# Optimization experiments

Hardware: AMD Instinct MI355X
Metric: run time of the kernel (lower is better)

The kernel has to match this reference:

```python
import jax, jax.numpy as jnp
import numpy as np

NU = 1.0  # degrees of freedom of the Student-t / Tsallis softmax


def setup_inputs() -> dict:
    key = jax.random.key(0)
    k1, k2, k3, k4 = jax.random.split(key, 4)
    B, Nx, Nh, Ny = 8192, 2048, 512, 1024
    x = jax.random.normal(k1, (B, Nx), dtype=jnp.float32)
    W_fc = jax.random.normal(k2, (Nh, Nx), dtype=jnp.float32) * (1.0 / np.sqrt(Nx))
    b_fc = jax.random.normal(k3, (Nh,), dtype=jnp.float32) * 0.01
    W_q = jax.random.normal(k4, (Ny, Nh), dtype=jnp.float32) * (1.0 / np.sqrt(Nh))
    return {"x": x, "W_fc": W_fc, "b_fc": b_fc, "W_q": W_q}


def reference(x, W_fc, b_fc, W_q):
    # x: [B, Nx] -> relu -> Linear(Nx, Nh) -> relu
    h = jax.nn.relu(jax.nn.relu(x) @ W_fc.T + b_fc)  # [B, Nh]
    # Quadratic layer: squared Euclidean distance to each class prototype.
    # ||h - w_j||^2 = ||h||^2 - 2 h.w_j + ||w_j||^2  (avoids [B, Ny, Nh] tensor)
    d = (jnp.sum(h * h, axis=-1, keepdims=True)
         - 2.0 * (h @ W_q.T)
         + jnp.sum(W_q * W_q, axis=-1))  # [B, Ny]
    d = jnp.maximum(d, 0.0)  # guard tiny negatives from fp cancellation
    # LogTSoftmax: p_j \propto (1 + d_j/nu)^{-(nu+1)/2}
    t = (-(NU + 1.0) / 2.0) * jnp.log1p(d / NU)  # [B, Ny]
    return t - jax.scipy.special.logsumexp(t, axis=-1, keepdims=True)
```

## Files before the change

kernel.cpp:

```cpp
#include <hip/hip_runtime.h>
#include <stdint.h>
#include <stddef.h>

#define B_ROWS 8192
#define NX 2048
#define NH 512
#define NY 1024

typedef __attribute__((ext_vector_type(8))) short bf16x8;
typedef __attribute__((ext_vector_type(4))) short bf16x4;
typedef __attribute__((ext_vector_type(4))) float f32x4;

static __device__ __forceinline__ unsigned short f2bf(float f) {
    union { float f; unsigned int u; } c; c.f = f;
    unsigned int r = 0x7FFFu + ((c.u >> 16) & 1u);
    return (unsigned short)((c.u + r) >> 16);
}
static __device__ __forceinline__ float bf2f(unsigned short b) {
    union { unsigned int u; float f; } c; c.u = ((unsigned int)b) << 16;
    return c.f;
}

static __device__ __forceinline__ void glld16(const void* g, void* l) {
    __builtin_amdgcn_global_load_lds(
        (const __attribute__((address_space(1))) unsigned int*)g,
        (__attribute__((address_space(3))) unsigned int*)l, 16, 0, 0);
}


__global__ __launch_bounds__(256) void cast_x_kernel(const float* __restrict__ x,
                                                     unsigned short* __restrict__ xb) {
    size_t idx = (size_t)(blockIdx.x * 256 + threadIdx.x) * 8;
    float4 a = *(const float4*)&x[idx];
    float4 b = *(const float4*)&x[idx + 4];
    bf16x8 o;
    o[0] = (short)f2bf(fmaxf(a.x, 0.f)); o[1] = (short)f2bf(fmaxf(a.y, 0.f));
    o[2] = (short)f2bf(fmaxf(a.z, 0.f)); o[3] = (short)f2bf(fmaxf(a.w, 0.f));
    o[4] = (short)f2bf(fmaxf(b.x, 0.f)); o[5] = (short)f2bf(fmaxf(b.y, 0.f));
    o[6] = (short)f2bf(fmaxf(b.z, 0.f)); o[7] = (short)f2bf(fmaxf(b.w, 0.f));
    *(bf16x8*)&xb[idx] = o;
}

__global__ __launch_bounds__(256) void cast_wfc_kernel(const float* __restrict__ w,
                                                       unsigned short* __restrict__ wb) {
    int idx = (blockIdx.x * 256 + threadIdx.x) * 4;
    float4 v = *(const float4*)&w[idx];
    bf16x4 o;
    o[0] = (short)f2bf(v.x); o[1] = (short)f2bf(v.y);
    o[2] = (short)f2bf(v.z); o[3] = (short)f2bf(v.w);
    *(bf16x4*)&wb[idx] = o;
}

__global__ __launch_bounds__(256) void prep_wq_kernel(const float* __restrict__ wq,
                                                      unsigned short* __restrict__ wqb,
                                                      float* __restrict__ wqsq) {
    int lane = threadIdx.x & 63;
    int row = blockIdx.x * 4 + (threadIdx.x >> 6);
    const float* p = wq + (size_t)row * NH + lane * 8;
    float4 a = *(const float4*)p;
    float4 b = *(const float4*)(p + 4);
    bf16x8 o;
    o[0] = (short)f2bf(a.x); o[1] = (short)f2bf(a.y);
    o[2] = (short)f2bf(a.z); o[3] = (short)f2bf(a.w);
    o[4] = (short)f2bf(b.x); o[5] = (short)f2bf(b.y);
    o[6] = (short)f2bf(b.z); o[7] = (short)f2bf(b.w);
    *(bf16x8*)&wqb[(size_t)row * NH + lane * 8] = o;
    float s = a.x*a.x + a.y*a.y + a.z*a.z + a.w*a.w
            + b.x*b.x + b.y*b.y + b.z*b.z + b.w*b.w;
    #pragma unroll
    for (int off = 32; off > 0; off >>= 1) s += __shfl_xor(s, off);
    if (lane == 0) wqsq[row] = s;
}

__global__ __launch_bounds__(256, 2) void gemm1_kernel(const unsigned short* __restrict__ xb,
                                                       const unsigned short* __restrict__ wfcb,
                                                       const float* __restrict__ b_fc,
                                                       unsigned short* __restrict__ hb) {
    __shared__ unsigned short As[64 * 64];
    __shared__ unsigned short Bs[128 * 64];

    const int tid = threadIdx.x;
    const int lane = tid & 63;
    const int wave = tid >> 6;
    const int wm = wave >> 1, wn = wave & 1;
    const int quad = lane >> 4;
    const int r = lane & 15;
    const int m0 = blockIdx.y * 64;
    const int n0 = blockIdx.x * 128;

    f32x4 acc[2][4];
    #pragma unroll
    for (int i = 0; i < 2; ++i)
        #pragma unroll
        for (int j = 0; j < 4; ++j) acc[i][j] = (f32x4)(0.0f);

    const int lrow = lane >> 3;
    const int gch = (lane & 7) ^ lrow;
    const char* xbB = (const char*)xb;
    const char* wfB = (const char*)wfcb;
    char* AsB = (char*)As;
    char* BsB = (char*)Bs;

    const int xk = r & 7;
    const int ch0 = ((quad) ^ xk) * 16;
    const int ch1 = ((4 + quad) ^ xk) * 16;
    const char* ardp = AsB + (wm * 32 + r) * 128;
    const char* brdp = BsB + (wn * 64 + r) * 128;

    for (int k0 = 0; k0 < NX; k0 += 64) {
        __syncthreads();
        #pragma unroll
        for (int c = 0; c < 2; ++c) {
            int R0 = wave * 16 + c * 8;
            glld16(xbB + (size_t)(m0 + R0 + lrow) * (NX * 2) + k0 * 2 + gch * 16,
                   AsB + R0 * 128);
        }
        #pragma unroll
        for (int c = 0; c < 4; ++c) {
            int R0 = wave * 32 + c * 8;
            glld16(wfB + (size_t)(n0 + R0 + lrow) * (NX * 2) + k0 * 2 + gch * 16,
                   BsB + R0 * 128);
        }
        __syncthreads();

        #pragma unroll
        for (int s = 0; s < 2; ++s) {
            const int ch = s ? ch1 : ch0;
            bf16x8 af[2], bfv[4];
            #pragma unroll
            for (int i = 0; i < 2; ++i) af[i] = *(const bf16x8*)(ardp + i * 16 * 128 + ch);
            #pragma unroll
            for (int j = 0; j < 4; ++j) bfv[j] = *(const bf16x8*)(brdp + j * 16 * 128 + ch);
            #pragma unroll
            for (int i = 0; i < 2; ++i)
                #pragma unroll
                for (int j = 0; j < 4; ++j)
                    acc[i][j] = __builtin_amdgcn_mfma_f32_16x16x32_bf16(af[i], bfv[j], acc[i][j], 0, 0, 0);
        }
    }

    #pragma unroll
    for (int i = 0; i < 2; ++i) {
        #pragma unroll
        for (int j = 0; j < 4; ++j) {
            int col = n0 + wn * 64 + j * 16 + r;
            float bias = b_fc[col];
            #pragma unroll
            for (int rr = 0; rr < 4; ++rr) {
                int row = m0 + wm * 32 + i * 16 + quad * 4 + rr;
                float v = fmaxf(acc[i][j][rr] + bias, 0.0f);
                hb[(size_t)row * NH + col] = f2bf(v);
            }
        }
    }
}

__global__ __launch_bounds__(256) void hsq_kernel(const unsigned short* __restrict__ hb,
                                                  float* __restrict__ hsq) {
    int lane = threadIdx.x & 63;
    int row = blockIdx.x * 4 + (threadIdx.x >> 6);
    bf16x8 v = *(const bf16x8*)&hb[(size_t)row * NH + lane * 8];
    float s = 0.f;
    #pragma unroll
    for (int i = 0; i < 8; ++i) {
        float f = bf2f((unsigned short)v[i]);
        s += f * f;
    }
    #pragma unroll
    for (int off = 32; off > 0; off >>= 1) s += __shfl_xor(s, off);
    if (lane == 0) hsq[row] = s;
}

__global__ __launch_bounds__(256, 2) void gemm2_kernel(const unsigned short* __restrict__ hb,
                                                       const unsigned short* __restrict__ wqb,
                                                       const float* __restrict__ hsq,
                                                       const float* __restrict__ wqsq,
                                                       float* __restrict__ out) {
    __shared__ unsigned short As[128 * 64];
    __shared__ unsigned short Bs[128 * 64];

    const int tid = threadIdx.x;
    const int lane = tid & 63;
    const int wave = tid >> 6;
    const int wm = wave >> 1, wn = wave & 1;
    const int quad = lane >> 4;
    const int r = lane & 15;
    const int m0 = blockIdx.y * 128;
    const int n0 = blockIdx.x * 128;

    f32x4 acc[4][4];
    #pragma unroll
    for (int i = 0; i < 4; ++i)
        #pragma unroll
        for (int j = 0; j < 4; ++j) acc[i][j] = (f32x4)(0.0f);

    const int lrow = lane >> 3;
    const int gch = (lane & 7) ^ lrow;
    const char* hbB = (const char*)hb;
    const char* wqB = (const char*)wqb;
    char* AsB = (char*)As;
    char* BsB = (char*)Bs;

    const int xk = r & 7;
    const int ch0 = ((quad) ^ xk) * 16;
    const int ch1 = ((4 + quad) ^ xk) * 16;
    const char* ardp = AsB + (wm * 64 + r) * 128;
    const char* brdp = BsB + (wn * 64 + r) * 128;

    for (int k0 = 0; k0 < NH; k0 += 64) {
        __syncthreads();
        #pragma unroll
        for (int c = 0; c < 4; ++c) {
            int R0 = wave * 32 + c * 8;
            glld16(hbB + (size_t)(m0 + R0 + lrow) * (NH * 2) + k0 * 2 + gch * 16,
                   AsB + R0 * 128);
            glld16(wqB + (size_t)(n0 + R0 + lrow) * (NH * 2) + k0 * 2 + gch * 16,
                   BsB + R0 * 128);
        }
        __syncthreads();

        #pragma unroll
        for (int s = 0; s < 2; ++s) {
            const int ch = s ? ch1 : ch0;
            bf16x8 af[4], bfv[4];
            #pragma unroll
            for (int i = 0; i < 4; ++i) af[i] = *(const bf16x8*)(ardp + i * 16 * 128 + ch);
            #pragma unroll
            for (int j = 0; j < 4; ++j) bfv[j] = *(const bf16x8*)(brdp + j * 16 * 128 + ch);
            #pragma unroll
            for (int i = 0; i < 4; ++i)
                #pragma unroll
                for (int j = 0; j < 4; ++j)
                    acc[i][j] = __builtin_amdgcn_mfma_f32_16x16x32_bf16(af[i], bfv[j], acc[i][j], 0, 0, 0);
        }
    }

    float hs[4][4];
    #pragma unroll
    for (int i = 0; i < 4; ++i)
        #pragma unroll
        for (int rr = 0; rr < 4; ++rr)
            hs[i][rr] = hsq[m0 + wm * 64 + i * 16 + quad * 4 + rr];

    #pragma unroll
    for (int i = 0; i < 4; ++i) {
        #pragma unroll
        for (int j = 0; j < 4; ++j) {
            int col = n0 + wn * 64 + j * 16 + r;
            float wq = wqsq[col];
            #pragma unroll
            for (int rr = 0; rr < 4; ++rr) {
                int row = m0 + wm * 64 + i * 16 + quad * 4 + rr;
                float d = hs[i][rr] - 2.0f * acc[i][j][rr] + wq;
                d = fmaxf(d, 0.0f);
                out[(size_t)row * NY + col] = -__logf(1.0f + d);
            }
        }
    }
}

__global__ __launch_bounds__(256) void lse_kernel(float* __restrict__ out) {
    __shared__ float redm[4];
    __shared__ float reds[4];
    const int tid = threadIdx.x;
    const int lane = tid & 63;
    const int wave = tid >> 6;
    float* p = out + (size_t)blockIdx.x * NY;
    float4 v = ((const float4*)p)[tid];
    float m = fmaxf(fmaxf(v.x, v.y), fmaxf(v.z, v.w));
    #pragma unroll
    for (int off = 32; off > 0; off >>= 1) m = fmaxf(m, __shfl_xor(m, off));
    if (lane == 0) redm[wave] = m;
    __syncthreads();
    m = fmaxf(fmaxf(redm[0], redm[1]), fmaxf(redm[2], redm[3]));
    float s = __expf(v.x - m) + __expf(v.y - m) + __expf(v.z - m) + __expf(v.w - m);
    #pragma unroll
    for (int off = 32; off > 0; off >>= 1) s += __shfl_xor(s, off);
    if (lane == 0) reds[wave] = s;
    __syncthreads();
    s = reds[0] + reds[1] + reds[2] + reds[3];
    float lse = m + __logf(s);
    v.x -= lse; v.y -= lse; v.z -= lse; v.w -= lse;
    ((float4*)p)[tid] = v;
}

extern "C" void kernel_launch(void* const* d_in, const int* in_sizes, int n_in,
                              void* d_out, int out_size, void* d_ws, size_t ws_size,
                              hipStream_t stream) {
    const float* x    = (const float*)d_in[0];
    const float* W_fc = (const float*)d_in[1];
    const float* b_fc = (const float*)d_in[2];
    const float* W_q  = (const float*)d_in[3];
    float* out = (float*)d_out;

    char* ws = (char*)d_ws;
    unsigned short* xb   = (unsigned short*)(ws);
    unsigned short* wfcb = (unsigned short*)(ws + 33554432);
    unsigned short* wqb  = (unsigned short*)(ws + 35651584);
    float*          wqsq = (float*)(ws + 36700160);
    unsigned short* hb   = (unsigned short*)(ws + 36704256);
    float*          hsq  = (float*)(ws + 45092864);

    cast_x_kernel<<<(B_ROWS * NX) / (256 * 8), 256, 0, stream>>>(x, xb);
    cast_wfc_kernel<<<(NH * NX) / (256 * 4), 256, 0, stream>>>(W_fc, wfcb);
    prep_wq_kernel<<<NY / 4, 256, 0, stream>>>(W_q, wqb, wqsq);
    gemm1_kernel<<<dim3(NH / 128, B_ROWS / 64), 256, 0, stream>>>(xb, wfcb, b_fc, hb);
    hsq_kernel<<<B_ROWS / 4, 256, 0, stream>>>(hb, hsq);
    gemm2_kernel<<<dim3(NY / 128, B_ROWS / 128), 256, 0, stream>>>(hb, wqb, hsq, wqsq, out);
    lse_kernel<<<B_ROWS, 256, 0, stream>>>(out);
}
```

Before: 183.0 us.

## Merge prep kernels, fuse row norms into GEMM1, deepen K tiles, simplify LSE

The three cast/prep kernels become one launch, and that launch also zeroes the hsq buffer. The ||h||^2 row sums are now accumulated in the GEMM1 epilogue with shuffles and atomicAdd, so the separate hsq kernel and its re-read of h go away. Both GEMMs now stage 128-wide K slices per barrier pair (doubling LDS per block), and GEMM1's launch bounds ask for 3 blocks per CU. The log-sum-exp drops its max reduction and one barrier, relying on all logits being non-positive. The costs are atomics, float rounding that now differs slightly from the bf16-rounded h, and higher LDS use that may limit occupancy.

```diff
diff --git a/kernel.cpp b/kernel.cpp
--- a/kernel.cpp
+++ b/kernel.cpp
@@ -7,6 +7,11 @@
 #define NH 512
 #define NY 1024
 
+#define X_ELEMS (B_ROWS * NX)
+#define EW_ELEMS (X_ELEMS + NH * NX)
+#define EW_BLOCKS (EW_ELEMS / (8 * 256))
+#define WQ_BLOCKS (NY / 4)
+
 typedef __attribute__((ext_vector_type(8))) short bf16x8;
 typedef __attribute__((ext_vector_type(4))) short bf16x4;
 typedef __attribute__((ext_vector_type(4))) float f32x4;
@@ -16,10 +21,6 @@
     unsigned int r = 0x7FFFu + ((c.u >> 16) & 1u);
     return (unsigned short)((c.u + r) >> 16);
 }
-static __device__ __forceinline__ float bf2f(unsigned short b) {
-    union { unsigned int u; float f; } c; c.u = ((unsigned int)b) << 16;
-    return c.f;
-}
 
 static __device__ __forceinline__ void glld16(const void* g, void* l) {
     __builtin_amdgcn_global_load_lds(
@@ -27,57 +28,67 @@
         (__attribute__((address_space(3))) unsigned int*)l, 16, 0, 0);
 }
 
-
-__global__ __launch_bounds__(256) void cast_x_kernel(const float* __restrict__ x,
-                                                     unsigned short* __restrict__ xb) {
-    size_t idx = (size_t)(blockIdx.x * 256 + threadIdx.x) * 8;
-    float4 a = *(const float4*)&x[idx];
-    float4 b = *(const float4*)&x[idx + 4];
-    bf16x8 o;
-    o[0] = (short)f2bf(fmaxf(a.x, 0.f)); o[1] = (short)f2bf(fmaxf(a.y, 0.f));
-    o[2] = (short)f2bf(fmaxf(a.z, 0.f)); o[3] = (short)f2bf(fmaxf(a.w, 0.f));
-    o[4] = (short)f2bf(fmaxf(b.x, 0.f)); o[5] = (short)f2bf(fmaxf(b.y, 0.f));
-    o[6] = (short)f2bf(fmaxf(b.z, 0.f)); o[7] = (short)f2bf(fmaxf(b.w, 0.f));
-    *(bf16x8*)&xb[idx] = o;
-}
-
-__global__ __launch_bounds__(256) void cast_wfc_kernel(const float* __restrict__ w,
-                                                       unsigned short* __restrict__ wb) {
-    int idx = (blockIdx.x * 256 + threadIdx.x) * 4;
-    float4 v = *(const float4*)&w[idx];
-    bf16x4 o;
-    o[0] = (short)f2bf(v.x); o[1] = (short)f2bf(v.y);
-    o[2] = (short)f2bf(v.z); o[3] = (short)f2bf(v.w);
-    *(bf16x4*)&wb[idx] = o;
-}
-
-__global__ __launch_bounds__(256) void prep_wq_kernel(const float* __restrict__ wq,
-                                                      unsigned short* __restrict__ wqb,
-                                                      float* __restrict__ wqsq) {
-    int lane = threadIdx.x & 63;
-    int row = blockIdx.x * 4 + (threadIdx.x >> 6);
-    const float* p = wq + (size_t)row * NH + lane * 8;
-    float4 a = *(const float4*)p;
-    float4 b = *(const float4*)(p + 4);
-    bf16x8 o;
-    o[0] = (short)f2bf(a.x); o[1] = (short)f2bf(a.y);
-    o[2] = (short)f2bf(a.z); o[3] = (short)f2bf(a.w);
-    o[4] = (short)f2bf(b.x); o[5] = (short)f2bf(b.y);
-    o[6] = (short)f2bf(b.z); o[7] = (short)f2bf(b.w);
-    *(bf16x8*)&wqb[(size_t)row * NH + lane * 8] = o;
-    float s = a.x*a.x + a.y*a.y + a.z*a.z + a.w*a.w
-            + b.x*b.x + b.y*b.y + b.z*b.z + b.w*b.w;
-    #pragma unroll
-    for (int off = 32; off > 0; off >>= 1) s += __shfl_xor(s, off);
-    if (lane == 0) wqsq[row] = s;
-}
-
-__global__ __launch_bounds__(256, 2) void gemm1_kernel(const unsigned short* __restrict__ xb,
+__global__ __launch_bounds__(256) void prep_kernel(const float* __restrict__ x,
+                                                   const float* __restrict__ wfc,
+                                                   const float* __restrict__ wq,
+                                                   unsigned short* __restrict__ xb,
+                                                   unsigned short* __restrict__ wfcb,
+                                                   unsigned short* __restrict__ wqb,
+                                                   float* __restrict__ wqsq,
+                                                   float* __restrict__ hsq) {
+    const int bid = blockIdx.x;
+    const int tid = threadIdx.x;
+    if (bid < EW_BLOCKS) {
+        size_t idx = ((size_t)bid * 256 + tid) * 8;
+        if (idx < (size_t)X_ELEMS) {
+            float4 a = *(const float4*)&x[idx];
+            float4 b = *(const float4*)&x[idx + 4];
+            bf16x8 o;
+            o[0] = (short)f2bf(fmaxf(a.x, 0.f)); o[1] = (short)f2bf(fmaxf(a.y, 0.f));
+            o[2] = (short)f2bf(fmaxf(a.z, 0.f)); o[3] = (short)f2bf(fmaxf(a.w, 0.f));
+            o[4] = (short)f2bf(fmaxf(b.x, 0.f)); o[5] = (short)f2bf(fmaxf(b.y, 0.f));
+            o[6] = (short)f2bf(fmaxf(b.z, 0.f)); o[7] = (short)f2bf(fmaxf(b.w, 0.f));
+            *(bf16x8*)&xb[idx] = o;
+        } else {
+            size_t off = idx - X_ELEMS;
+            float4 a = *(const float4*)&wfc[off];
+            float4 b = *(const float4*)&wfc[off + 4];
+            bf16x8 o;
+            o[0] = (short)f2bf(a.x); o[1] = (short)f2bf(a.y);
+            o[2] = (short)f2bf(a.z); o[3] = (short)f2bf(a.w);
+            o[4] = (short)f2bf(b.x); o[5] = (short)f2bf(b.y);
+            o[6] = (short)f2bf(b.z); o[7] = (short)f2bf(b.w);
+            *(bf16x8*)&wfcb[off] = o;
+        }
+    } else {
+        const int b2 = bid - EW_BLOCKS;
+        const int lane = tid & 63;
+        const int row = b2 * 4 + (tid >> 6);
+        const float* p = wq + (size_t)row * NH + lane * 8;
+        float4 a = *(const float4*)p;
+        float4 b = *(const float4*)(p + 4);
+        bf16x8 o;
+        o[0] = (short)f2bf(a.x); o[1] = (short)f2bf(a.y);
+        o[2] = (short)f2bf(a.z); o[3] = (short)f2bf(a.w);
+        o[4] = (short)f2bf(b.x); o[5] = (short)f2bf(b.y);
+        o[6] = (short)f2bf(b.z); o[7] = (short)f2bf(b.w);
+        *(bf16x8*)&wqb[(size_t)row * NH + lane * 8] = o;
+        float s = a.x*a.x + a.y*a.y + a.z*a.z + a.w*a.w
+                + b.x*b.x + b.y*b.y + b.z*b.z + b.w*b.w;
+        #pragma unroll
+        for (int off = 32; off > 0; off >>= 1) s += __shfl_xor(s, off);
+        if (lane == 0) wqsq[row] = s;
+        if (tid < 32) hsq[b2 * 32 + tid] = 0.0f;
+    }
+}
+
+__global__ __launch_bounds__(256, 3) void gemm1_kernel(const unsigned short* __restrict__ xb,
                                                        const unsigned short* __restrict__ wfcb,
                                                        const float* __restrict__ b_fc,
-                                                       unsigned short* __restrict__ hb) {
-    __shared__ unsigned short As[64 * 64];
-    __shared__ unsigned short Bs[128 * 64];
+                                                       unsigned short* __restrict__ hb,
+                                                       float* __restrict__ hsq) {
+    __shared__ unsigned short As[2 * 64 * 64];
+    __shared__ unsigned short Bs[2 * 128 * 64];
 
     const int tid = threadIdx.x;
     const int lane = tid & 63;
@@ -107,37 +118,52 @@
     const char* ardp = AsB + (wm * 32 + r) * 128;
     const char* brdp = BsB + (wn * 64 + r) * 128;
 
-    for (int k0 = 0; k0 < NX; k0 += 64) {
+    for (int k0 = 0; k0 < NX; k0 += 128) {
         __syncthreads();
         #pragma unroll
-        for (int c = 0; c < 2; ++c) {
-            int R0 = wave * 16 + c * 8;
-            glld16(xbB + (size_t)(m0 + R0 + lrow) * (NX * 2) + k0 * 2 + gch * 16,
-                   AsB + R0 * 128);
-        }
-        #pragma unroll
-        for (int c = 0; c < 4; ++c) {
-            int R0 = wave * 32 + c * 8;
-            glld16(wfB + (size_t)(n0 + R0 + lrow) * (NX * 2) + k0 * 2 + gch * 16,
-                   BsB + R0 * 128);
+        for (int t = 0; t < 2; ++t) {
+            const int kk = (k0 + t * 64) * 2;
+            #pragma unroll
+            for (int c = 0; c < 2; ++c) {
+                int R0 = wave * 16 + c * 8;
+                glld16(xbB + (size_t)(m0 + R0 + lrow) * (NX * 2) + kk + gch * 16,
+                       AsB + t * 8192 + R0 * 128);
+            }
+            #pragma unroll
+            for (int c = 0; c < 4; ++c) {
+                int R0 = wave * 32 + c * 8;
+                glld16(wfB + (size_t)(n0 + R0 + lrow) * (NX * 2) + kk + gch * 16,
+                       BsB + t * 16384 + R0 * 128);
+            }
         }
         __syncthreads();
 
         #pragma unroll
-        for (int s = 0; s < 2; ++s) {
-            const int ch = s ? ch1 : ch0;
-            bf16x8 af[2], bfv[4];
-            #pragma unroll
-            for (int i = 0; i < 2; ++i) af[i] = *(const bf16x8*)(ardp + i * 16 * 128 + ch);
-            #pragma unroll
-            for (int j = 0; j < 4; ++j) bfv[j] = *(const bf16x8*)(brdp + j * 16 * 128 + ch);
-            #pragma unroll
-            for (int i = 0; i < 2; ++i)
-                #pragma unroll
-                for (int j = 0; j < 4; ++j)
-                    acc[i][j] = __builtin_amdgcn_mfma_f32_16x16x32_bf16(af[i], bfv[j], acc[i][j], 0, 0, 0);
-        }
-    }
+        for (int t = 0; t < 2; ++t) {
+            #pragma unroll
+            for (int s = 0; s < 2; ++s) {
+                const int ch = (s ? ch1 : ch0) + t * 0;
+                const char* ap = ardp + t * 8192;
+                const char* bp = brdp + t * 16384;
+                bf16x8 af[2], bfv[4];
+                #pragma unroll
+                for (int i = 0; i < 2; ++i) af[i] = *(const bf16x8*)(ap + i * 16 * 128 + ch);
+                #pragma unroll
+                for (int j = 0; j < 4; ++j) bfv[j] = *(const bf16x8*)(bp + j * 16 * 128 + ch);
+                #pragma unroll
+                for (int i = 0; i < 2; ++i)
+                    #pragma unroll
+                    for (int j = 0; j < 4; ++j)
+                        acc[i][j] = __builtin_amdgcn_mfma_f32_16x16x32_bf16(af[i], bfv[j], acc[i][j], 0, 0, 0);
+            }
+        }
+    }
+
+    float p[2][4];
+    #pragma unroll
+    for (int i = 0; i < 2; ++i)
+        #pragma unroll
+        for (int rr = 0; rr < 4; ++rr) p[i][rr] = 0.0f;
 
     #pragma unroll
     for (int i = 0; i < 2; ++i) {
@@ -150,25 +176,25 @@
                 int row = m0 + wm * 32 + i * 16 + quad * 4 + rr;
                 float v = fmaxf(acc[i][j][rr] + bias, 0.0f);
                 hb[(size_t)row * NH + col] = f2bf(v);
-            }
-        }
-    }
-}
-
-__global__ __launch_bounds__(256) void hsq_kernel(const unsigned short* __restrict__ hb,
-                                                  float* __restrict__ hsq) {
-    int lane = threadIdx.x & 63;
-    int row = blockIdx.x * 4 + (threadIdx.x >> 6);
-    bf16x8 v = *(const bf16x8*)&hb[(size_t)row * NH + lane * 8];
-    float s = 0.f;
-    #pragma unroll
-    for (int i = 0; i < 8; ++i) {
-        float f = bf2f((unsigned short)v[i]);
-        s += f * f;
-    }
-    #pragma unroll
-    for (int off = 32; off > 0; off >>= 1) s += __shfl_xor(s, off);
-    if (lane == 0) hsq[row] = s;
+                p[i][rr] += v * v;
+            }
+        }
+    }
+    #pragma unroll
+    for (int mask = 1; mask < 16; mask <<= 1) {
+        #pragma unroll
+        for (int i = 0; i < 2; ++i)
+            #pragma unroll
+            for (int rr = 0; rr < 4; ++rr)
+                p[i][rr] += __shfl_xor(p[i][rr], mask);
+    }
+    if (r == 0) {
+        #pragma unroll
+        for (int i = 0; i < 2; ++i)
+            #pragma unroll
+            for (int rr = 0; rr < 4; ++rr)
+                atomicAdd(&hsq[m0 + wm * 32 + i * 16 + quad * 4 + rr], p[i][rr]);
+    }
 }
 
 __global__ __launch_bounds__(256, 2) void gemm2_kernel(const unsigned short* __restrict__ hb,
@@ -176,8 +202,8 @@
                                                        const float* __restrict__ hsq,
                                                        const float* __restrict__ wqsq,
                                                        float* __restrict__ out) {
-    __shared__ unsigned short As[128 * 64];
-    __shared__ unsigned short Bs[128 * 64];
+    __shared__ unsigned short As[2 * 128 * 64];
+    __shared__ unsigned short Bs[2 * 128 * 64];
 
     const int tid = threadIdx.x;
     const int lane = tid & 63;
@@ -207,31 +233,40 @@
     const char* ardp = AsB + (wm * 64 + r) * 128;
     const char* brdp = BsB + (wn * 64 + r) * 128;
 
-    for (int k0 = 0; k0 < NH; k0 += 64) {
+    for (int k0 = 0; k0 < NH; k0 += 128) {
         __syncthreads();
         #pragma unroll
-        for (int c = 0; c < 4; ++c) {
-            int R0 = wave * 32 + c * 8;
-            glld16(hbB + (size_t)(m0 + R0 + lrow) * (NH * 2) + k0 * 2 + gch * 16,
-                   AsB + R0 * 128);
-            glld16(wqB + (size_t)(n0 + R0 + lrow) * (NH * 2) + k0 * 2 + gch * 16,
-                   BsB + R0 * 128);
+        for (int t = 0; t < 2; ++t) {
+            const int kk = (k0 + t * 64) * 2;
+            #pragma unroll
+            for (int c = 0; c < 4; ++c) {
+                int R0 = wave * 32 + c * 8;
+                glld16(hbB + (size_t)(m0 + R0 + lrow) * (NH * 2) + kk + gch * 16,
+                       AsB + t * 16384 + R0 * 128);
+                glld16(wqB + (size_t)(n0 + R0 + lrow) * (NH * 2) + kk + gch * 16,
+                       BsB + t * 16384 + R0 * 128);
+            }
         }
         __syncthreads();
 
         #pragma unroll
-        for (int s = 0; s < 2; ++s) {
-            const int ch = s ? ch1 : ch0;
-            bf16x8 af[4], bfv[4];
-            #pragma unroll
-            for (int i = 0; i < 4; ++i) af[i] = *(const bf16x8*)(ardp + i * 16 * 128 + ch);
-            #pragma unroll
-            for (int j = 0; j < 4; ++j) bfv[j] = *(const bf16x8*)(brdp + j * 16 * 128 + ch);
-            #pragma unroll
-            for (int i = 0; i < 4; ++i)
-                #pragma unroll
-                for (int j = 0; j < 4; ++j)
-                    acc[i][j] = __builtin_amdgcn_mfma_f32_16x16x32_bf16(af[i], bfv[j], acc[i][j], 0, 0, 0);
+        for (int t = 0; t < 2; ++t) {
+            #pragma unroll
+            for (int s = 0; s < 2; ++s) {
+                const int ch = s ? ch1 : ch0;
+                const char* ap = ardp + t * 16384;
+                const char* bp = brdp + t * 16384;
+                bf16x8 af[4], bfv[4];
+                #pragma unroll
+                for (int i = 0; i < 4; ++i) af[i] = *(const bf16x8*)(ap + i * 16 * 128 + ch);
+                #pragma unroll
+                for (int j = 0; j < 4; ++j) bfv[j] = *(const bf16x8*)(bp + j * 16 * 128 + ch);
+                #pragma unroll
+                for (int i = 0; i < 4; ++i)
+                    #pragma unroll
+                    for (int j = 0; j < 4; ++j)
+                        acc[i][j] = __builtin_amdgcn_mfma_f32_16x16x32_bf16(af[i], bfv[j], acc[i][j], 0, 0, 0);
+            }
         }
     }
 
@@ -260,26 +295,18 @@
 }
 
 __global__ __launch_bounds__(256) void lse_kernel(float* __restrict__ out) {
-    __shared__ float redm[4];
     __shared__ float reds[4];
     const int tid = threadIdx.x;
     const int lane = tid & 63;
     const int wave = tid >> 6;
     float* p = out + (size_t)blockIdx.x * NY;
     float4 v = ((const float4*)p)[tid];
-    float m = fmaxf(fmaxf(v.x, v.y), fmaxf(v.z, v.w));
-    #pragma unroll
-    for (int off = 32; off > 0; off >>= 1) m = fmaxf(m, __shfl_xor(m, off));
-    if (lane == 0) redm[wave] = m;
-    __syncthreads();
-    m = fmaxf(fmaxf(redm[0], redm[1]), fmaxf(redm[2], redm[3]));
-    float s = __expf(v.x - m) + __expf(v.y - m) + __expf(v.z - m) + __expf(v.w - m);
+    float s = __expf(v.x) + __expf(v.y) + __expf(v.z) + __expf(v.w);
     #pragma unroll
     for (int off = 32; off > 0; off >>= 1) s += __shfl_xor(s, off);
     if (lane == 0) reds[wave] = s;
     __syncthreads();
-    s = reds[0] + reds[1] + reds[2] + reds[3];
-    float lse = m + __logf(s);
+    float lse = __logf(reds[0] + reds[1] + reds[2] + reds[3]);
     v.x -= lse; v.y -= lse; v.z -= lse; v.w -= lse;
     ((float4*)p)[tid] = v;
 }
@@ -301,11 +328,8 @@
     unsigned short* hb   = (unsigned short*)(ws + 36704256);
     float*          hsq  = (float*)(ws + 45092864);
 
-    cast_x_kernel<<<(B_ROWS * NX) / (256 * 8), 256, 0, stream>>>(x, xb);
-    cast_wfc_kernel<<<(NH * NX) / (256 * 4), 256, 0, stream>>>(W_fc, wfcb);
-    prep_wq_kernel<<<NY / 4, 256, 0, stream>>>(W_q, wqb, wqsq);
-    gemm1_kernel<<<dim3(NH / 128, B_ROWS / 64), 256, 0, stream>>>(xb, wfcb, b_fc, hb);
-    hsq_kernel<<<B_ROWS / 4, 256, 0, stream>>>(hb, hsq);
+    prep_kernel<<<EW_BLOCKS + WQ_BLOCKS, 256, 0, stream>>>(x, W_fc, W_q, xb, wfcb, wqb, wqsq, hsq);
+    gemm1_kernel<<<dim3(NH / 128, B_ROWS / 64), 256, 0, stream>>>(xb, wfcb, b_fc, hb, hsq);
     gemm2_kernel<<<dim3(NY / 128, B_ROWS / 128), 256, 0, stream>>>(hb, wqb, hsq, wqsq, out);
     lse_kernel<<<B_ROWS, 256, 0, stream>>>(out);
 }
```

Result: faster. 179.3 us (-2.0%).
